# Kernel tuning notes

Hardware: AMD Instinct MI355X
Metric: run time of the kernel (lower is better)

## Reference

```python
import jax, jax.numpy as jnp
import numpy as np

N, S, EMB, H = 8, 1024, 512, 8
D = EMB // H  # head_dim = 64


def setup_inputs() -> dict:
    key = jax.random.key(0)
    ks = jax.random.split(key, 12)
    f = lambda k_, shp, s=1.0: jax.random.normal(k_, shp, dtype=jnp.float32) * s
    return {
        "v": f(ks[0], (N, S, EMB)),
        "k": f(ks[1], (N, S, EMB)),
        "q": f(ks[2], (N, S, EMB)),
        "Wv": f(ks[3], (D, D), 0.02), "bv": jnp.zeros((D,), jnp.float32),
        "Wk": f(ks[4], (D, D), 0.02), "bk": jnp.zeros((D,), jnp.float32),
        "Wq": f(ks[5], (D, D), 0.02), "bq": jnp.zeros((D,), jnp.float32),
        "E": f(ks[6], (1, S, D), 0.02),   # relative-position embedding
        "Wo": f(ks[7], (EMB, EMB), 0.02), "bo": jnp.zeros((EMB,), jnp.float32),
    }


def reference(v, k, q, Wv, bv, Wk, bk, Wq, bq, E, Wo, bo):
    n = v.shape[0]
    # per-head linear projections (module == 'spatiotemporal' branch)
    vals = v.reshape(n, S, H, D) @ Wv.T + bv   # (n,S,H,D)
    keys = k.reshape(n, S, H, D) @ Wk.T + bk
    qrs = q.reshape(n, S, H, D) @ Wq.T + bq

    # relative-position bias via skew trick (uses VALUES, as in source)
    QE = jnp.einsum('nlhd,sd->nhls', vals, E[0])            # (n,H,S,S)
    flip_mask = jnp.flip(jnp.triu(jnp.ones((S, S), bool), 1), axis=1)
    QE = jnp.where(flip_mask, 0.0, QE)                      # _mask_positions
    padded = jnp.pad(QE, ((0, 0), (0, 0), (0, 0), (1, 0)))  # left-pad last dim
    Sbias = padded.reshape(n, H, S + 1, S)[:, :, 1:, :]     # _skew -> (n,H,S,S)

    # attention scores with the source's mask semantics:
    # masked_fill(mask == 0, -1e20) keeps entries where triu(...,1) == 1
    qk = jnp.einsum('nqhd,nkhd->nhqk', qrs, keys)           # (n,H,S,S)
    keep = jnp.triu(jnp.ones((S, S), bool), 1)
    qk = jnp.where(keep, qk, jnp.float32(-1e20))

    attn = jax.nn.softmax(qk / jnp.sqrt(jnp.float32(EMB)), axis=3) + Sbias

    z = jnp.einsum('nhql,nlhd->nqhd', attn, vals).reshape(n, S, EMB)
    return z @ Wo.T + bo
```

## Files before the change

### kernel.cpp

```cpp
#include <hip/hip_runtime.h>
#include <hip/hip_bf16.h>

#define SDIM 1024
#define HNUM 8
#define DDIM 64
#define EMBD 512
#define NBATCH 8

static constexpr float SCALE = 0.044194173824159216f;

typedef short bf16x8 __attribute__((ext_vector_type(8)));
typedef float f32x4 __attribute__((ext_vector_type(4)));

__device__ __forceinline__ ushort bf16_of(float f) {
    return __builtin_bit_cast(unsigned short, __float2bfloat16(f));
}
__device__ __forceinline__ float f32_of(ushort u) {
    return __bfloat162float(__builtin_bit_cast(__hip_bfloat16, u));
}

__device__ __forceinline__ bf16x8 lds8(const ushort* base, int row, int slot) {
    return *(const bf16x8*)(base + (row * 8 + (slot ^ (row & 7))) * 8);
}

#define MFMA(a, b, c) __builtin_amdgcn_mfma_f32_16x16x32_bf16(a, b, c, 0, 0, 0)

__global__ __launch_bounds__(256) void proj_mfma(
    const float* __restrict__ xv, const float* __restrict__ xk, const float* __restrict__ xq,
    const float* __restrict__ Wv, const float* __restrict__ bv,
    const float* __restrict__ Wk, const float* __restrict__ bk,
    const float* __restrict__ Wq, const float* __restrict__ bq,
    ushort* __restrict__ vals_bf, ushort* __restrict__ keys_bf, ushort* __restrict__ qrs_bf)
{
    __shared__ ushort a_s[256 * 64];
    __shared__ ushort w_s[64 * 64];

    const int blk = blockIdx.x;
    const int m = blk % 3;
    const int chunk = blk / 3;
    const int tok0 = chunk * 32;
    const int n = tok0 >> 10, s0 = tok0 & 1023;
    const int t = threadIdx.x;
    const int w = t >> 6, l = t & 63, lrow = l & 15, lgrp = l >> 4;

    const float* X = (m == 0) ? xv : (m == 1) ? xk : xq;
    const float* W = (m == 0) ? Wv : (m == 1) ? Wk : Wq;
    const float* B = (m == 0) ? bv : (m == 1) ? bk : bq;
    ushort* O = (m == 0) ? vals_bf : (m == 1) ? keys_bf : qrs_bf;

    #pragma unroll
    for (int i = 0; i < 16; ++i) {
        const int f4 = i * 256 + t;
        const int ls = f4 >> 7, c4 = f4 & 127;
        const int h = c4 >> 4, d4 = c4 & 15;
        const float4 v = ((const float4*)(X + (size_t)(tok0 + ls) * EMBD))[c4];
        ushort4 u;
        u.x = bf16_of(v.x); u.y = bf16_of(v.y); u.z = bf16_of(v.z); u.w = bf16_of(v.w);
        const int r = h * 32 + ls, slot = d4 >> 1;
        *(ushort4*)(a_s + (r * 8 + (slot ^ (r & 7))) * 8 + (d4 & 1) * 4) = u;
    }
    #pragma unroll
    for (int i = 0; i < 4; ++i) {
        const int f4 = i * 256 + t;
        const int r = f4 >> 4, d4 = f4 & 15;
        const float4 v = ((const float4*)W)[f4];
        ushort4 u;
        u.x = bf16_of(v.x); u.y = bf16_of(v.y); u.z = bf16_of(v.z); u.w = bf16_of(v.w);
        const int slot = d4 >> 1;
        *(ushort4*)(w_s + (r * 8 + (slot ^ (r & 7))) * 8 + (d4 & 1) * 4) = u;
    }
    __syncthreads();

    f32x4 acc[4][4];
    #pragma unroll
    for (int fr = 0; fr < 4; ++fr)
        #pragma unroll
        for (int fc = 0; fc < 4; ++fc) acc[fr][fc] = {0.f, 0.f, 0.f, 0.f};

    bf16x8 af[4][2];
    #pragma unroll
    for (int fr = 0; fr < 4; ++fr)
        #pragma unroll
        for (int kc = 0; kc < 2; ++kc)
            af[fr][kc] = lds8(a_s, w * 64 + fr * 16 + lrow, lgrp + kc * 4);

    #pragma unroll
    for (int fc = 0; fc < 4; ++fc)
        #pragma unroll
        for (int kc = 0; kc < 2; ++kc) {
            const bf16x8 bfr = lds8(w_s, fc * 16 + lrow, lgrp + kc * 4);
            #pragma unroll
            for (int fr = 0; fr < 4; ++fr)
                acc[fr][fc] = MFMA(af[fr][kc], bfr, acc[fr][fc]);
        }
    __syncthreads();

    float bias[4];
    #pragma unroll
    for (int fc = 0; fc < 4; ++fc) bias[fc] = B[fc * 16 + lrow];
    #pragma unroll
    for (int fr = 0; fr < 4; ++fr)
        #pragma unroll
        for (int fc = 0; fc < 4; ++fc)
            #pragma unroll
            for (int reg = 0; reg < 4; ++reg) {
                const int row = w * 64 + fr * 16 + lgrp * 4 + reg;
                const int col = fc * 16 + lrow;
                a_s[(row * 8 + ((col >> 3) ^ (row & 7))) * 8 + (col & 7)] =
                    bf16_of(acc[fr][fc][reg] + bias[fc]);
            }
    __syncthreads();

    #pragma unroll
    for (int i = 0; i < 8; ++i) {
        const int cc = i * 256 + t;
        const int r = cc >> 3, slot = cc & 7;
        const int h = r >> 5, ls = r & 31;
        const float4 v = *(const float4*)(a_s + (r * 8 + (slot ^ (r & 7))) * 8);
        *(float4*)(O + ((size_t)(n * HNUM + h) * SDIM + s0 + ls) * DDIM + slot * 8) = v;
    }
}

__global__ __launch_bounds__(256) void conv_e(const float* __restrict__ E, ushort* __restrict__ e_bf) {
    const int i = blockIdx.x * 256 + threadIdx.x;
    e_bf[i] = bf16_of(E[i]);
}
__global__ __launch_bounds__(256) void conv_wo(const float* __restrict__ Wo, ushort* __restrict__ wo_bf) {
    const int i = blockIdx.x * 256 + threadIdx.x;
    wo_bf[i] = bf16_of(Wo[i]);
}

__global__ __launch_bounds__(256) void transpose_vals(
    const ushort* __restrict__ vals_bf, ushort* __restrict__ valsT_bf)
{
    __shared__ ushort tile[64][72];
    const int blk = blockIdx.x;
    const int st = blk & 15, nh = blk >> 4;
    const int s0 = st * 64;
    const int t = threadIdx.x;
    const ushort* src = vals_bf + (nh * SDIM + s0) * DDIM;
    #pragma unroll
    for (int i = 0; i < 2; ++i) {
        const int c = t + i * 256;
        const int row = c >> 3, slot = c & 7;
        const float4 vv = ((const float4*)src)[c];
        *(float4*)&tile[row][slot * 8] = vv;
    }
    __syncthreads();
    const int d = t >> 2, si = (t & 3) * 16;
    union { ushort u[16]; float4 f[2]; } buf;
    #pragma unroll
    for (int u2 = 0; u2 < 16; ++u2) buf.u[u2] = tile[si + u2][d];
    float4* dst = (float4*)(valsT_bf + (nh * DDIM + d) * SDIM + s0 + si);
    dst[0] = buf.f[0];
    dst[1] = buf.f[1];
}

__global__ __launch_bounds__(256, 2) void attn_mfma(
    const ushort* __restrict__ vals_bf, const ushort* __restrict__ keys_bf,
    const ushort* __restrict__ qrs_bf, const ushort* __restrict__ valsT_bf,
    const ushort* __restrict__ e_bf, ushort* __restrict__ zh)
{
    __shared__ ushort kbuf [2][64 * 64];
    __shared__ ushort vtbuf[2][64 * 64];
    __shared__ ushort p_s[64 * 64];

    const int vid = blockIdx.x;
    const int blk = (vid & 7) * 128 + (vid >> 3);
    const int rg = blk & 15, h = (blk >> 4) & 7, n = blk >> 7;
    const int i0 = rg * 64;
    const int t = threadIdx.x;
    const int w = t >> 6, l = t & 63, lrow = l & 15, lgrp = l >> 4;

    const ushort* Qb  = qrs_bf   + (n * HNUM + h) * (SDIM * DDIM);
    const ushort* Kb  = keys_bf  + (n * HNUM + h) * (SDIM * DDIM);
    const ushort* Vb  = vals_bf  + (n * HNUM + h) * (SDIM * DDIM);
    const ushort* VTb = valsT_bf + (n * HNUM + h) * (SDIM * DDIM);

    const int grow0 = i0 + w * 16 + lrow;
    const bool lastw = (rg == 15 && w == 3);

    bf16x8 a_q[2], a_vi[2];
    #pragma unroll
    for (int kc = 0; kc < 2; ++kc) {
        a_q[kc]  = *(const bf16x8*)(Qb + grow0 * DDIM + kc * 32 + lgrp * 8);
        a_vi[kc] = *(const bf16x8*)(Vb + grow0 * DDIM + kc * 32 + lgrp * 8);
    }

    f32x4 accn[4], accz[4];
    #pragma unroll
    for (int f = 0; f < 4; ++f) {
        accn[f] = {0.f, 0.f, 0.f, 0.f};
        accz[f] = {0.f, 0.f, 0.f, 0.f};
    }
    float den[4] = {0.f, 0.f, 0.f, 0.f};
    float vsum[4] = {0.f, 0.f, 0.f, 0.f};

    const int sr0 = t >> 3, sr1 = (t >> 3) + 32, ss = t & 7;
    const int sw0 = (sr0 * 8 + (ss ^ (sr0 & 7))) * 8;
    const int sw1 = (sr1 * 8 + (ss ^ (sr1 & 7))) * 8;

    {
        const float4 v0 = *(const float4*)(VTb + sr0 * SDIM + ss * 8);
        const float4 v1 = *(const float4*)(VTb + sr1 * SDIM + ss * 8);
        *(float4*)(vtbuf[0] + sw0) = v0;
        *(float4*)(vtbuf[0] + sw1) = v1;
        if (rg == 0) {
            const float4 k0 = *(const float4*)(Kb + sr0 * DDIM + ss * 8);
            const float4 k1 = *(const float4*)(Kb + sr1 * DDIM + ss * 8);
            *(float4*)(kbuf[0] + sw0) = k0;
            *(float4*)(kbuf[0] + sw1) = k1;
        }
    }
    __syncthreads();

    for (int jt = 0; jt < 16; ++jt) {
        const int cur = jt & 1, nxt = cur ^ 1;
        const int j0 = jt * 64;
        const bool diag = (jt == rg);
        const ushort* vt_s = vtbuf[cur];
        const ushort* k_s  = kbuf[cur];

        float4 nv0, nv1, nk0, nk1;
        const bool stgK = (jt < 15) && (jt + 1 >= rg);
        if (jt < 15) {
            nv0 = *(const float4*)(VTb + sr0 * SDIM + j0 + 64 + ss * 8);
            nv1 = *(const float4*)(VTb + sr1 * SDIM + j0 + 64 + ss * 8);
        }
        if (stgK) {
            nk0 = *(const float4*)(Kb + (j0 + 64 + sr0) * DDIM + ss * 8);
            nk1 = *(const float4*)(Kb + (j0 + 64 + sr1) * DDIM + ss * 8);
        }

        if (jt <= rg) {
            const int eb = SDIM - 64 - i0 + j0;
            #pragma unroll
            for (int half = 0; half < 2; ++half) {
                f32x4 bd[4];
                #pragma unroll
                for (int fq = 0; fq < 4; ++fq) bd[fq] = {0.f, 0.f, 0.f, 0.f};
                #pragma unroll
                for (int fq = 0; fq < 4; ++fq) {
                    const int fc = half * 4 + fq;
                    if (fc + w >= 3 && fc + w <= 7) {
                        const int g = eb + fc * 16 + lrow;
                        #pragma unroll
                        for (int kc = 0; kc < 2; ++kc) {
                            bf16x8 ef = {0, 0, 0, 0, 0, 0, 0, 0};
                            if (g < SDIM)
                                ef = *(const bf16x8*)(e_bf + g * DDIM + kc * 32 + lgrp * 8);
                            bd[fq] = MFMA(a_vi[kc], ef, bd[fq]);
                        }
                    }
                }
                #pragma unroll
                for (int fq = 0; fq < 4; ++fq) {
                    const int fc = half * 4 + fq;
                    if (fc + w >= 3 && fc + w <= 7) {
                        const int u = fc * 16 + lrow;
                        #pragma unroll
                        for (int r = 0; r < 4; ++r) {
                            const int rs = w * 16 + lgrp * 4 + r;
                            const int c = u - 63 + rs;
                            if (c >= 0 && c < 64)
                                p_s[(rs * 8 + ((c >> 3) ^ (rs & 7))) * 8 + (c & 7)] = bf16_of(bd[fq][r]);
                        }
                    }
                }
            }
            {
                bf16x8 ap[2];
                #pragma unroll
                for (int kc = 0; kc < 2; ++kc) ap[kc] = lds8(p_s, w * 16 + lrow, lgrp + kc * 4);
                __builtin_amdgcn_s_setprio(1);
                #pragma unroll
                for (int fc = 0; fc < 4; ++fc) {
                    #pragma unroll
                    for (int kc = 0; kc < 2; ++kc) {
                        const bf16x8 vt = lds8(vt_s, fc * 16 + lrow, lgrp + kc * 4);
                        accz[fc] = MFMA(ap[kc], vt, accz[fc]);
                        if (lastw)
                            #pragma unroll
                            for (int u = 0; u < 8; ++u) vsum[fc] += f32_of((ushort)vt[u]);
                    }
                }
                __builtin_amdgcn_s_setprio(0);
            }
        }

        if (jt >= rg) {
            f32x4 sf[4];
            #pragma unroll
            for (int fc = 0; fc < 4; ++fc) sf[fc] = {0.f, 0.f, 0.f, 0.f};
            __builtin_amdgcn_s_setprio(1);
            #pragma unroll
            for (int fc = 0; fc < 4; ++fc)
                if (!diag || fc >= w)
                    #pragma unroll
                    for (int kc = 0; kc < 2; ++kc)
                        sf[fc] = MFMA(a_q[kc], lds8(k_s, fc * 16 + lrow, lgrp + kc * 4), sf[fc]);
            __builtin_amdgcn_s_setprio(0);
            #pragma unroll
            for (int fc = 0; fc < 4; ++fc) {
                #pragma unroll
                for (int r = 0; r < 4; ++r) {
                    const int rs = w * 16 + lgrp * 4 + r;
                    const int col = fc * 16 + lrow;
                    float e = 0.f;
                    if (!diag || col > rs) e = __expf(sf[fc][r] * SCALE);
                    den[r] += e;
                    p_s[(rs * 8 + ((col >> 3) ^ (rs & 7))) * 8 + (col & 7)] = bf16_of(e);
                }
            }
            {
                bf16x8 ap[2];
                #pragma unroll
                for (int kc = 0; kc < 2; ++kc) ap[kc] = lds8(p_s, w * 16 + lrow, lgrp + kc * 4);
                __builtin_amdgcn_s_setprio(1);
                #pragma unroll
                for (int fc = 0; fc < 4; ++fc)
                    #pragma unroll
                    for (int kc = 0; kc < 2; ++kc)
                        accn[fc] = MFMA(ap[kc], lds8(vt_s, fc * 16 + lrow, lgrp + kc * 4), accn[fc]);
                __builtin_amdgcn_s_setprio(0);
            }
        }

        if (jt < 15) {
            *(float4*)(vtbuf[nxt] + sw0) = nv0;
            *(float4*)(vtbuf[nxt] + sw1) = nv1;
            if (stgK) {
                *(float4*)(kbuf[nxt] + sw0) = nk0;
                *(float4*)(kbuf[nxt] + sw1) = nk1;
            }
            __syncthreads();
        }
    }

    #pragma unroll
    for (int r = 0; r < 4; ++r) {
        float d = den[r];
        d += __shfl_xor(d, 1);
        d += __shfl_xor(d, 2);
        d += __shfl_xor(d, 4);
        d += __shfl_xor(d, 8);
        den[r] = d;
    }
    float vsr[4];
    #pragma unroll
    for (int fc = 0; fc < 4; ++fc) {
        float vv = vsum[fc];
        vv += __shfl_xor(vv, 16);
        vv += __shfl_xor(vv, 32);
        vsr[fc] = vv;
    }

    #pragma unroll
    for (int fc = 0; fc < 4; ++fc) {
        #pragma unroll
        for (int r = 0; r < 4; ++r) {
            const int grow = i0 + w * 16 + lgrp * 4 + r;
            const int col = fc * 16 + lrow;
            float o;
            if (grow == SDIM - 1)
                o = vsr[fc] * (1.0f / SDIM) + accz[fc][r];
            else
                o = accn[fc][r] / den[r] + accz[fc][r];
            zh[(size_t)(n * SDIM + grow) * EMBD + h * DDIM + col] = bf16_of(o);
        }
    }
}

__global__ __launch_bounds__(256) void out_mfma(
    const ushort* __restrict__ zh, const ushort* __restrict__ wo_bf,
    const float* __restrict__ bo, float* __restrict__ out)
{
    __shared__ ushort ah_s[128 * 64];
    __shared__ ushort b_s [64 * 64];

    const int vid = blockIdx.x;
    const int blk = (vid & 7) * 64 + (vid >> 3);
    const int r0 = (blk >> 3) * 128, c0 = (blk & 7) * 64;
    const int t = threadIdx.x;
    const int w = t >> 6, l = t & 63, lrow = l & 15, lgrp = l >> 4;

    f32x4 acc[2][4];
    #pragma unroll
    for (int fr = 0; fr < 2; ++fr)
        #pragma unroll
        for (int fc = 0; fc < 4; ++fc) acc[fr][fc] = {0.f, 0.f, 0.f, 0.f};

    for (int kt = 0; kt < 8; ++kt) {
        __syncthreads();
        #pragma unroll
        for (int i = 0; i < 4; ++i) {
            const int cc = i * 256 + t;
            const int r = cc >> 3, slot = cc & 7;
            const size_t src = (size_t)(r0 + r) * EMBD + kt * 64 + slot * 8;
            *(float4*)(ah_s + (r * 8 + (slot ^ (r & 7))) * 8) = *(const float4*)(zh + src);
        }
        #pragma unroll
        for (int i = 0; i < 2; ++i) {
            const int cc = i * 256 + t;
            const int r = cc >> 3, slot = cc & 7;
            const float4 vb = *(const float4*)(wo_bf + (size_t)(c0 + r) * EMBD + kt * 64 + slot * 8);
            *(float4*)(b_s + (r * 8 + (slot ^ (r & 7))) * 8) = vb;
        }
        __syncthreads();

        #pragma unroll
        for (int kc = 0; kc < 2; ++kc)
            #pragma unroll
            for (int fc = 0; fc < 4; ++fc) {
                const bf16x8 bfr = lds8(b_s, fc * 16 + lrow, lgrp + kc * 4);
                #pragma unroll
                for (int fr = 0; fr < 2; ++fr)
                    acc[fr][fc] = MFMA(lds8(ah_s, w * 32 + fr * 16 + lrow, lgrp + kc * 4), bfr, acc[fr][fc]);
            }
    }

    float bias[4];
    #pragma unroll
    for (int fc = 0; fc < 4; ++fc) bias[fc] = bo[c0 + fc * 16 + lrow];
    #pragma unroll
    for (int fr = 0; fr < 2; ++fr)
        #pragma unroll
        for (int fc = 0; fc < 4; ++fc)
            #pragma unroll
            for (int reg = 0; reg < 4; ++reg) {
                const int row = r0 + w * 32 + fr * 16 + lgrp * 4 + reg;
                const int col = c0 + fc * 16 + lrow;
                out[(size_t)row * EMBD + col] = acc[fr][fc][reg] + bias[fc];
            }
}

extern "C" void kernel_launch(void* const* d_in, const int* in_sizes, int n_in,
                              void* d_out, int out_size, void* d_ws, size_t ws_size,
                              hipStream_t stream) {
    const float* v  = (const float*)d_in[0];
    const float* k  = (const float*)d_in[1];
    const float* q  = (const float*)d_in[2];
    const float* Wv = (const float*)d_in[3];
    const float* bv = (const float*)d_in[4];
    const float* Wk = (const float*)d_in[5];
    const float* bk = (const float*)d_in[6];
    const float* Wq = (const float*)d_in[7];
    const float* bq = (const float*)d_in[8];
    const float* E  = (const float*)d_in[9];
    const float* Wo = (const float*)d_in[10];
    const float* bo = (const float*)d_in[11];
    float* out = (float*)d_out;

    char* ws = (char*)d_ws;
    ushort* qrs_bf   = (ushort*)(ws);
    ushort* keys_bf  = (ushort*)(ws + ((size_t)8 << 20));
    ushort* vals_bf  = (ushort*)(ws + ((size_t)16 << 20));
    ushort* valsT_bf = (ushort*)(ws + ((size_t)24 << 20));
    ushort* e_bf     = (ushort*)(ws + ((size_t)32 << 20));
    ushort* wo_bf    = (ushort*)(ws + ((size_t)33 << 20));
    ushort* zh       = (ushort*)(ws + ((size_t)34 << 20));

    proj_mfma<<<768, 256, 0, stream>>>(v, k, q, Wv, bv, Wk, bk, Wq, bq,
                                       vals_bf, keys_bf, qrs_bf);
    conv_e<<<(SDIM * DDIM) / 256, 256, 0, stream>>>(E, e_bf);
    conv_wo<<<(EMBD * EMBD) / 256, 256, 0, stream>>>(Wo, wo_bf);
    transpose_vals<<<NBATCH * HNUM * 16, 256, 0, stream>>>(vals_bf, valsT_bf);
    attn_mfma<<<NBATCH * HNUM * 16, 256, 0, stream>>>(vals_bf, keys_bf, qrs_bf,
                                                      valsT_bf, e_bf, zh);
    out_mfma<<<512, 256, 0, stream>>>(zh, wo_bf, bo, out);
}
```

Baseline: 129.6 us.

## Fuse V transpose into projection and widen attention blocks to 128 query rows

```diff
diff --git a/kernel.cpp b/kernel.cpp
--- a/kernel.cpp
+++ b/kernel.cpp
@@ -30,7 +30,8 @@
     const float* __restrict__ Wv, const float* __restrict__ bv,
     const float* __restrict__ Wk, const float* __restrict__ bk,
     const float* __restrict__ Wq, const float* __restrict__ bq,
-    ushort* __restrict__ vals_bf, ushort* __restrict__ keys_bf, ushort* __restrict__ qrs_bf)
+    ushort* __restrict__ vals_bf, ushort* __restrict__ keys_bf, ushort* __restrict__ qrs_bf,
+    ushort* __restrict__ valsT_bf)
 {
     __shared__ ushort a_s[256 * 64];
     __shared__ ushort w_s[64 * 64];
@@ -119,6 +120,22 @@
         const float4 v = *(const float4*)(a_s + (r * 8 + (slot ^ (r & 7))) * 8);
         *(float4*)(O + ((size_t)(n * HNUM + h) * SDIM + s0 + ls) * DDIM + slot * 8) = v;
     }
+
+    if (m == 0) {
+        #pragma unroll
+        for (int i = 0; i < 2; ++i) {
+            const int cid = i * 256 + t;
+            const int hh = cid >> 6, d = cid & 63;
+            union { ushort u[32]; float4 f[4]; } col;
+            #pragma unroll
+            for (int ls = 0; ls < 32; ++ls) {
+                const int r = hh * 32 + ls;
+                col.u[ls] = a_s[(r * 8 + ((d >> 3) ^ (r & 7))) * 8 + (d & 7)];
+            }
+            float4* dst = (float4*)(valsT_bf + ((size_t)(n * HNUM + hh) * DDIM + d) * SDIM + s0);
+            dst[0] = col.f[0]; dst[1] = col.f[1]; dst[2] = col.f[2]; dst[3] = col.f[3];
+        }
+    }
 }
 
 __global__ __launch_bounds__(256) void conv_e(const float* __restrict__ E, ushort* __restrict__ e_bf) {
@@ -130,47 +147,24 @@
     wo_bf[i] = bf16_of(Wo[i]);
 }
 
-__global__ __launch_bounds__(256) void transpose_vals(
-    const ushort* __restrict__ vals_bf, ushort* __restrict__ valsT_bf)
-{
-    __shared__ ushort tile[64][72];
-    const int blk = blockIdx.x;
-    const int st = blk & 15, nh = blk >> 4;
-    const int s0 = st * 64;
-    const int t = threadIdx.x;
-    const ushort* src = vals_bf + (nh * SDIM + s0) * DDIM;
-    #pragma unroll
-    for (int i = 0; i < 2; ++i) {
-        const int c = t + i * 256;
-        const int row = c >> 3, slot = c & 7;
-        const float4 vv = ((const float4*)src)[c];
-        *(float4*)&tile[row][slot * 8] = vv;
-    }
-    __syncthreads();
-    const int d = t >> 2, si = (t & 3) * 16;
-    union { ushort u[16]; float4 f[2]; } buf;
-    #pragma unroll
-    for (int u2 = 0; u2 < 16; ++u2) buf.u[u2] = tile[si + u2][d];
-    float4* dst = (float4*)(valsT_bf + (nh * DDIM + d) * SDIM + s0 + si);
-    dst[0] = buf.f[0];
-    dst[1] = buf.f[1];
-}
-
-__global__ __launch_bounds__(256, 2) void attn_mfma(
+__global__ __launch_bounds__(512, 2) void attn_mfma(
     const ushort* __restrict__ vals_bf, const ushort* __restrict__ keys_bf,
     const ushort* __restrict__ qrs_bf, const ushort* __restrict__ valsT_bf,
     const ushort* __restrict__ e_bf, ushort* __restrict__ zh)
 {
     __shared__ ushort kbuf [2][64 * 64];
     __shared__ ushort vtbuf[2][64 * 64];
-    __shared__ ushort p_s[64 * 64];
+    __shared__ ushort p_s[128 * 64];
 
     const int vid = blockIdx.x;
-    const int blk = (vid & 7) * 128 + (vid >> 3);
-    const int rg = blk & 15, h = (blk >> 4) & 7, n = blk >> 7;
-    const int i0 = rg * 64;
+    const int blk = (vid & 7) * 64 + (vid >> 3);
+    const int bt = blk & 7, h = (blk >> 3) & 7, n = blk >> 6;
+    const int i0 = bt * 128;
     const int t = threadIdx.x;
     const int w = t >> 6, l = t & 63, lrow = l & 15, lgrp = l >> 4;
+    const int s = w >> 2, q = w & 3;
+    const int myit = 2 * bt + s;
+    const int i0s = i0 + s * 64;
 
     const ushort* Qb  = qrs_bf   + (n * HNUM + h) * (SDIM * DDIM);
     const ushort* Kb  = keys_bf  + (n * HNUM + h) * (SDIM * DDIM);
@@ -178,7 +172,7 @@
     const ushort* VTb = valsT_bf + (n * HNUM + h) * (SDIM * DDIM);
 
     const int grow0 = i0 + w * 16 + lrow;
-    const bool lastw = (rg == 15 && w == 3);
+    const bool lastw = (bt == 7 && w == 7);
 
     bf16x8 a_q[2], a_vi[2];
     #pragma unroll
@@ -196,44 +190,32 @@
     float den[4] = {0.f, 0.f, 0.f, 0.f};
     float vsum[4] = {0.f, 0.f, 0.f, 0.f};
 
-    const int sr0 = t >> 3, sr1 = (t >> 3) + 32, ss = t & 7;
-    const int sw0 = (sr0 * 8 + (ss ^ (sr0 & 7))) * 8;
-    const int sw1 = (sr1 * 8 + (ss ^ (sr1 & 7))) * 8;
+    const int srow = t >> 3, sslot = t & 7;
+    const int sw = (srow * 8 + (sslot ^ (srow & 7))) * 8;
 
     {
-        const float4 v0 = *(const float4*)(VTb + sr0 * SDIM + ss * 8);
-        const float4 v1 = *(const float4*)(VTb + sr1 * SDIM + ss * 8);
-        *(float4*)(vtbuf[0] + sw0) = v0;
-        *(float4*)(vtbuf[0] + sw1) = v1;
-        if (rg == 0) {
-            const float4 k0 = *(const float4*)(Kb + sr0 * DDIM + ss * 8);
-            const float4 k1 = *(const float4*)(Kb + sr1 * DDIM + ss * 8);
-            *(float4*)(kbuf[0] + sw0) = k0;
-            *(float4*)(kbuf[0] + sw1) = k1;
-        }
+        *(float4*)(vtbuf[0] + sw) = *(const float4*)(VTb + srow * SDIM + sslot * 8);
+        if (bt == 0)
+            *(float4*)(kbuf[0] + sw) = *(const float4*)(Kb + srow * DDIM + sslot * 8);
     }
     __syncthreads();
 
     for (int jt = 0; jt < 16; ++jt) {
         const int cur = jt & 1, nxt = cur ^ 1;
         const int j0 = jt * 64;
-        const bool diag = (jt == rg);
+        const bool diag = (jt == myit);
         const ushort* vt_s = vtbuf[cur];
         const ushort* k_s  = kbuf[cur];
 
-        float4 nv0, nv1, nk0, nk1;
-        const bool stgK = (jt < 15) && (jt + 1 >= rg);
-        if (jt < 15) {
-            nv0 = *(const float4*)(VTb + sr0 * SDIM + j0 + 64 + ss * 8);
-            nv1 = *(const float4*)(VTb + sr1 * SDIM + j0 + 64 + ss * 8);
-        }
-        if (stgK) {
-            nk0 = *(const float4*)(Kb + (j0 + 64 + sr0) * DDIM + ss * 8);
-            nk1 = *(const float4*)(Kb + (j0 + 64 + sr1) * DDIM + ss * 8);
-        }
-
-        if (jt <= rg) {
-            const int eb = SDIM - 64 - i0 + j0;
+        float4 nv, nk;
+        const bool stgK = (jt < 15) && (jt + 1 >= 2 * bt);
+        if (jt < 15)
+            nv = *(const float4*)(VTb + srow * SDIM + j0 + 64 + sslot * 8);
+        if (stgK)
+            nk = *(const float4*)(Kb + (j0 + 64 + srow) * DDIM + sslot * 8);
+
+        if (jt <= myit) {
+            const int eb = SDIM - 64 - i0s + j0;
             #pragma unroll
             for (int half = 0; half < 2; ++half) {
                 f32x4 bd[4];
@@ -242,7 +224,7 @@
                 #pragma unroll
                 for (int fq = 0; fq < 4; ++fq) {
                     const int fc = half * 4 + fq;
-                    if (fc + w >= 3 && fc + w <= 7) {
+                    if (fc + q >= 3 && fc + q <= 7) {
                         const int g = eb + fc * 16 + lrow;
                         #pragma unroll
                         for (int kc = 0; kc < 2; ++kc) {
@@ -256,14 +238,16 @@
                 #pragma unroll
                 for (int fq = 0; fq < 4; ++fq) {
                     const int fc = half * 4 + fq;
-                    if (fc + w >= 3 && fc + w <= 7) {
+                    if (fc + q >= 3 && fc + q <= 7) {
                         const int u = fc * 16 + lrow;
                         #pragma unroll
                         for (int r = 0; r < 4; ++r) {
-                            const int rs = w * 16 + lgrp * 4 + r;
+                            const int rs = q * 16 + lgrp * 4 + r;
                             const int c = u - 63 + rs;
-                            if (c >= 0 && c < 64)
-                                p_s[(rs * 8 + ((c >> 3) ^ (rs & 7))) * 8 + (c & 7)] = bf16_of(bd[fq][r]);
+                            if (c >= 0 && c < 64) {
+                                const int prow = w * 16 + lgrp * 4 + r;
+                                p_s[(prow * 8 + ((c >> 3) ^ (prow & 7))) * 8 + (c & 7)] = bf16_of(bd[fq][r]);
+                            }
                         }
                     }
                 }
@@ -288,14 +272,14 @@
             }
         }
 
-        if (jt >= rg) {
+        if (jt >= myit) {
             f32x4 sf[4];
             #pragma unroll
             for (int fc = 0; fc < 4; ++fc) sf[fc] = {0.f, 0.f, 0.f, 0.f};
             __builtin_amdgcn_s_setprio(1);
             #pragma unroll
             for (int fc = 0; fc < 4; ++fc)
-                if (!diag || fc >= w)
+                if (!diag || fc >= q)
                     #pragma unroll
                     for (int kc = 0; kc < 2; ++kc)
                         sf[fc] = MFMA(a_q[kc], lds8(k_s, fc * 16 + lrow, lgrp + kc * 4), sf[fc]);
@@ -304,12 +288,13 @@
             for (int fc = 0; fc < 4; ++fc) {
                 #pragma unroll
                 for (int r = 0; r < 4; ++r) {
-                    const int rs = w * 16 + lgrp * 4 + r;
+                    const int rs = q * 16 + lgrp * 4 + r;
                     const int col = fc * 16 + lrow;
                     float e = 0.f;
                     if (!diag || col > rs) e = __expf(sf[fc][r] * SCALE);
                     den[r] += e;
-                    p_s[(rs * 8 + ((col >> 3) ^ (rs & 7))) * 8 + (col & 7)] = bf16_of(e);
+                    const int prow = w * 16 + lgrp * 4 + r;
+                    p_s[(prow * 8 + ((col >> 3) ^ (prow & 7))) * 8 + (col & 7)] = bf16_of(e);
                 }
             }
             {
@@ -327,12 +312,9 @@
         }
 
         if (jt < 15) {
-            *(float4*)(vtbuf[nxt] + sw0) = nv0;
-            *(float4*)(vtbuf[nxt] + sw1) = nv1;
-            if (stgK) {
-                *(float4*)(kbuf[nxt] + sw0) = nk0;
-                *(float4*)(kbuf[nxt] + sw1) = nk1;
-            }
+            *(float4*)(vtbuf[nxt] + sw) = nv;
+            if (stgK)
+                *(float4*)(kbuf[nxt] + sw) = nk;
             __syncthreads();
         }
     }
@@ -461,11 +443,10 @@
     ushort* zh       = (ushort*)(ws + ((size_t)34 << 20));
 
     proj_mfma<<<768, 256, 0, stream>>>(v, k, q, Wv, bv, Wk, bk, Wq, bq,
-                                       vals_bf, keys_bf, qrs_bf);
+                                       vals_bf, keys_bf, qrs_bf, valsT_bf);
     conv_e<<<(SDIM * DDIM) / 256, 256, 0, stream>>>(E, e_bf);
     conv_wo<<<(EMBD * EMBD) / 256, 256, 0, stream>>>(Wo, wo_bf);
-    transpose_vals<<<NBATCH * HNUM * 16, 256, 0, stream>>>(vals_bf, valsT_bf);
-    attn_mfma<<<NBATCH * HNUM * 16, 256, 0, stream>>>(vals_bf, keys_bf, qrs_bf,
-                                                      valsT_bf, e_bf, zh);
+    attn_mfma<<<512, 512, 0, stream>>>(vals_bf, keys_bf, qrs_bf,
+                                       valsT_bf, e_bf, zh);
     out_mfma<<<512, 256, 0, stream>>>(zh, wo_bf, bo, out);
 }
```

After: 146.5 us. 1.13x slower.
